# Kernel tuning notes

Hardware: AMD Instinct MI355X
Metric: run time of the kernel (lower is better)

## Reference

```python
import jax, jax.numpy as jnp
import numpy as np

K = 8          # branching factor
D = 4          # tree depth (leaves at depth D)
H = 32         # const node dim
LEAVES = K ** D  # 4096
B = 32
OUT = 2
EPS = 1e-5


def _layer_dims(d):
    # depth d layer: in = (#units at depth d+1), out = (#nodes at d) * H
    n = K ** d
    in_per_child = H if d < D - 1 else 1  # leaf layer feeds scalars
    return n, n * K * in_per_child, n * H, in_per_child


def setup_inputs() -> dict:
    key = jax.random.key(0)
    ks = jax.random.split(key, 64)
    inp = {"x": jax.random.normal(ks[0], (B, LEAVES), jnp.float32)}
    i = 1
    for d in range(D - 1, -1, -1):
        n, fin, fout, ipc = _layer_dims(d)
        # block-diagonal pruning mask: node j rows <- its K children's blocks
        mask = jnp.asarray(np.kron(np.eye(n, dtype=np.float32),
                                   np.ones((H, K * ipc), dtype=np.float32)))
        s = 1.0 / np.sqrt(fin)
        inp[f"Wm{d}"] = jax.random.uniform(ks[i], (fout, fin), jnp.float32, -s, s) * mask; i += 1
        inp[f"bm{d}"] = jax.random.uniform(ks[i], (fout,), jnp.float32, -s, s); i += 1
        inp[f"Wl{d}"] = jax.random.uniform(ks[i], (fout, fin), jnp.float32, -s, s) * mask; i += 1
        inp[f"bl{d}"] = jax.random.uniform(ks[i], (fout,), jnp.float32, -s, s); i += 1
    inp["gate"] = jnp.float32(0.3)
    inp["bn_gamma"] = jnp.ones((H,), jnp.float32)
    inp["bn_beta"] = jnp.zeros((H,), jnp.float32)
    so = 1.0 / np.sqrt(H)
    inp["Wout"] = jax.random.uniform(ks[i], (OUT, H), jnp.float32, -so, so); i += 1
    inp["bout"] = jax.random.uniform(ks[i], (OUT,), jnp.float32, -so, so)
    return inp


def reference(x, Wm3, bm3, Wl3, bl3, Wm2, bm2, Wl2, bl2,
              Wm1, bm1, Wl1, bl1, Wm0, bm0, Wl0, bl0,
              gate, bn_gamma, bn_beta, Wout, bout):
    x_linear = x
    layers = ((Wm3, bm3, Wl3, bl3), (Wm2, bm2, Wl2, bl2),
              (Wm1, bm1, Wl1, bl1), (Wm0, bm0, Wl0, bl0))
    for Wm, bm, Wl, bl in layers:  # depth D-1 -> 0, as in torch forward
        h = jax.nn.relu(x @ Wm.T + bm)          # mlp branch (masked weights)
        x_linear = x_linear @ Wl.T + bl          # parallel linear branch
        x = h * gate + (1.0 - gate) * x_linear   # gated residual combine
    # BatchNorm1d in training mode (biased batch variance)
    mu = jnp.mean(x, axis=0)
    var = jnp.var(x, axis=0)
    xn = (x - mu) * jax.lax.rsqrt(var + EPS)
    y = xn * bn_gamma + bn_beta
    return y @ Wout.T + bout
```

## Files before the change

kernel.cpp:

```cpp
#include <hip/hip_runtime.h>


#define MAGIC 0x5CA1AB1E

__device__ __forceinline__ float dot4(float4 a, float4 b, float acc) {
    acc = fmaf(a.x, b.x, acc);
    acc = fmaf(a.y, b.y, acc);
    acc = fmaf(a.z, b.z, acc);
    acc = fmaf(a.w, b.w, acc);
    return acc;
}
__device__ __forceinline__ float4 ld4(const float* p) { return *(const float4*)p; }

typedef const __attribute__((address_space(1))) void* gas_t;
typedef __attribute__((address_space(3))) void* las_t;

__device__ __forceinline__ void gl_lds16(const float* g, float* l) {
    __builtin_amdgcn_global_load_lds((gas_t)g, (las_t)l, 16, 0, 0);
}

__device__ __forceinline__ void st_xch2(float2* p, float a, float b) {
    union { float2 f2; unsigned long long u; } v;
    v.f2 = make_float2(a, b);
    (void)atomicExch((unsigned long long*)p, v.u);
}
__device__ __forceinline__ float2 ld_wt2(const float2* p) {
    union { float2 f2; unsigned long long u; } v;
    v.u = __hip_atomic_load((const unsigned long long*)p,
                            __ATOMIC_RELAXED, __HIP_MEMORY_SCOPE_AGENT);
    return v.f2;
}
__device__ __forceinline__ void flag_set(int* p) {
    __atomic_signal_fence(__ATOMIC_SEQ_CST);
    __hip_atomic_store(p, MAGIC, __ATOMIC_RELAXED, __HIP_MEMORY_SCOPE_AGENT);
}
__device__ __forceinline__ void flag_wait(const int* p) {
    while (__hip_atomic_load(p, __ATOMIC_RELAXED, __HIP_MEMORY_SCOPE_AGENT) != MAGIC) {}
    __atomic_signal_fence(__ATOMIC_SEQ_CST);
}

__global__ __launch_bounds__(512)
void fused_tree(const float* __restrict__ x,
                const float* __restrict__ Wm3, const float* __restrict__ bm3,
                const float* __restrict__ Wl3, const float* __restrict__ bl3,
                const float* __restrict__ Wm2, const float* __restrict__ bm2,
                const float* __restrict__ Wl2, const float* __restrict__ bl2,
                const float* __restrict__ Wm1, const float* __restrict__ bm1,
                const float* __restrict__ Wl1, const float* __restrict__ bl1,
                const float* __restrict__ Wm0, const float* __restrict__ bm0,
                const float* __restrict__ Wl0, const float* __restrict__ bl0,
                const float* __restrict__ gate_p,
                const float* __restrict__ bn_gamma, const float* __restrict__ bn_beta,
                const float* __restrict__ Wout, const float* __restrict__ bout,
                float2* __restrict__ Qml, float2* __restrict__ Pml,
                int* __restrict__ flags1, int* __restrict__ flags2,
                float* __restrict__ out)
{
    const int blk = blockIdx.x;
    const int j2 = blk & 63, rg = blk >> 6;
    const int tid = threadIdx.x;
    const int wv = tid >> 6, ln = tid & 63;
    const int j1 = j2 >> 3, s = j2 & 7;
    const int cid = rg * 8 + j1;
    const bool is_consumer = (s == 0);

    __shared__ __align__(16) float w2[2][32][260];
    __shared__ __align__(16) float x3[8][260];
    __shared__ __align__(16) float xl3[8][260];
    __shared__ __align__(16) float x2s[8][36];
    __shared__ __align__(16) float xl2s[8][36];
    __shared__ __align__(16) float qm_own[8][36];
    __shared__ __align__(16) float ql_own[8][36];
    __shared__ __align__(16) float x1s[8][36];
    __shared__ __align__(16) float xl1s[8][36];
    __shared__ float x0s[32][33];
    __shared__ float bnm[32], bna[32];
    __shared__ float pW[64], pbo[2], pg[32], pb[32], pbm0[32], pbl0[32];

    const int col = tid & 255, hh3 = tid >> 8;
    const int l3 = col >> 5, t3 = col & 31;
    const int j3 = j2 * 8 + l3;
    const int row3 = j3 * 32 + t3;

    float4 xra[4], xrb[4];
#pragma unroll
    for (int i = 0; i < 4; ++i) {
        const float* xp = x + (size_t)(rg * 8 + hh3 * 4 + i) * 4096 + j3 * 8;
        xra[i] = ld4(xp);
        xrb[i] = ld4(xp + 4);
    }
    const float* wmr = Wm3 + (size_t)row3 * 4096 + j3 * 8;
    const float* wlr = Wl3 + (size_t)row3 * 4096 + j3 * 8;
    const float4 wma = ld4(wmr), wmb = ld4(wmr + 4);
    const float4 wla = ld4(wlr), wlb = ld4(wlr + 4);
    const float bm3v = bm3[row3], bl3v = bl3[row3];
    const float g = gate_p[0], gi = 1.0f - g;

    __builtin_amdgcn_sched_barrier(0);

#pragma unroll
    for (int i = 0; i < 8; ++i) {
        const int q = wv * 8 + i;
        const int m = q >> 5, r = q & 31;
        const float* src = (m ? Wl2 : Wm2)
                         + (size_t)(j2 * 32 + r) * 16384 + j2 * 256 + ln * 4;
        gl_lds16(src, &w2[m][r][0]);
    }
    __builtin_amdgcn_sched_barrier(0);

    const int t2 = tid >> 4;
    const float bm2v = bm2[j2 * 32 + t2];
    const float bl2v = bl2[j2 * 32 + t2];

    const int hp = tid & 1;
    float4 wm1r[4], wl1r[4];
    {
        const float* wr = Wm1 + (size_t)(j1 * 32 + t2) * 2048 + j2 * 32 + hp * 16;
        const float* lr = Wl1 + (size_t)(j1 * 32 + t2) * 2048 + j2 * 32 + hp * 16;
#pragma unroll
        for (int k = 0; k < 4; ++k) {
            wm1r[k] = ld4(wr + k * 4);
            wl1r[k] = ld4(lr + k * 4);
        }
    }

    float4 wm0r[4], wl0r[4];
    float bm1v = 0.0f, bl1v = 0.0f;
    if (is_consumer) {
        const int o2 = tid >> 4;
        const float* p0 = Wm0 + o2 * 256 + j1 * 32 + hp * 16;
        const float* p1 = Wl0 + o2 * 256 + j1 * 32 + hp * 16;
#pragma unroll
        for (int k = 0; k < 4; ++k) {
            wm0r[k] = ld4(p0 + k * 4);
            wl0r[k] = ld4(p1 + k * 4);
        }
        if (tid < 256) {
            bm1v = bm1[j1 * 32 + (tid & 31)];
            bl1v = bl1[j1 * 32 + (tid & 31)];
        }
    }
    if (blk == 0) {
        if (tid < 64) pW[tid] = Wout[tid];
        if (tid < 32) {
            pg[tid]   = bn_gamma[tid];
            pb[tid]   = bn_beta[tid];
            pbm0[tid] = bm0[tid];
            pbl0[tid] = bl0[tid];
        }
        if (tid < 2) pbo[tid] = bout[tid];
    }

#pragma unroll
    for (int i = 0; i < 4; ++i) {
        const int b = hh3 * 4 + i;
        float am = dot4(xra[i], wma, bm3v); am = dot4(xrb[i], wmb, am);
        float al = dot4(xra[i], wla, bl3v); al = dot4(xrb[i], wlb, al);
        x3[b][col]  = fmaf(g, fmaxf(am, 0.0f), gi * al);
        xl3[b][col] = al;
    }
    __syncthreads();

    {
        const int b = (tid >> 1) & 7;
        const float* wmp = &w2[0][t2][hp * 128];
        const float* wlp = &w2[1][t2][hp * 128];
        float pm = 0.0f, pl = 0.0f;
#pragma unroll 8
        for (int c = 0; c < 128; c += 4) {
            pm = dot4(ld4(&x3 [b][hp * 128 + c]), ld4(wmp + c), pm);
            pl = dot4(ld4(&xl3[b][hp * 128 + c]), ld4(wlp + c), pl);
        }
        pm += __shfl_xor(pm, 1);
        pl += __shfl_xor(pl, 1);
        const float am = pm + bm2v, al = pl + bl2v;
        if (hp == 0) x2s [b][t2] = fmaf(g, fmaxf(am, 0.0f), gi * al);
        else         xl2s[b][t2] = al;
    }
    __syncthreads();

    {
        const int b = (tid >> 1) & 7;
        const float* xp = &x2s [b][hp * 16];
        const float* xq = &xl2s[b][hp * 16];
        float pm = 0.0f, pl = 0.0f;
#pragma unroll
        for (int k = 0; k < 4; ++k) {
            pm = dot4(ld4(xp + k * 4), wm1r[k], pm);
            pl = dot4(ld4(xq + k * 4), wl1r[k], pl);
        }
        pm += __shfl_xor(pm, 1);
        pl += __shfl_xor(pl, 1);
        if (is_consumer) {
            if (hp == 0) { qm_own[b][t2] = pm; ql_own[b][t2] = pl; }
        } else if (hp == 0) {
            st_xch2(&Qml[((cid * 8 + s) * 8 + b) * 32 + t2], pm, pl);
        }
    }
    __syncthreads();
    if (!is_consumer) {
        if (tid == 0) flag_set(&flags1[cid * 8 + s]);
        return;
    }

    if (tid < 7) flag_wait(&flags1[cid * 8 + 1 + tid]);
    __syncthreads();

    if (tid < 256) {
        const int b = tid >> 5, t1 = tid & 31;
        float am = bm1v + qm_own[b][t1];
        float al = bl1v + ql_own[b][t1];
#pragma unroll
        for (int t = 1; t < 8; ++t) {
            const float2 q = ld_wt2(&Qml[((cid * 8 + t) * 8 + b) * 32 + t1]);
            am += q.x;
            al += q.y;
        }
        x1s [b][t1] = fmaf(g, fmaxf(am, 0.0f), gi * al);
        xl1s[b][t1] = al;
    }
    __syncthreads();

    {
        const int o2 = tid >> 4, b = (tid >> 1) & 7;
        float pm0 = 0.0f, pl0 = 0.0f;
#pragma unroll
        for (int k = 0; k < 4; ++k) {
            pm0 = dot4(ld4(&x1s [b][hp * 16 + k * 4]), wm0r[k], pm0);
            pl0 = dot4(ld4(&xl1s[b][hp * 16 + k * 4]), wl0r[k], pl0);
        }
        pm0 += __shfl_xor(pm0, 1);
        pl0 += __shfl_xor(pl0, 1);
        if (hp == 0)
            st_xch2(&Pml[j1 * 1024 + (rg * 8 + b) * 32 + o2], pm0, pl0);
    }
    __syncthreads();
    if (blk != 0) {
        if (tid == 0) flag_set(&flags2[cid]);
        return;
    }

    if (tid < 31) flag_wait(&flags2[tid + 1]);
    __syncthreads();

    for (int i = tid; i < 1024; i += 512) {
        const int r = i >> 5, o = i & 31;
        float am = pbm0[o], al = pbl0[o];
#pragma unroll
        for (int j = 0; j < 8; ++j) {
            const float2 p = ld_wt2(&Pml[j * 1024 + r * 32 + o]);
            am += p.x;
            al += p.y;
        }
        x0s[r][o] = fmaf(g, fmaxf(am, 0.0f), gi * al);
    }
    __syncthreads();

    if (tid < 32) {
        float sum = 0.0f, s2 = 0.0f;
#pragma unroll
        for (int r = 0; r < 32; ++r) {
            const float v = x0s[r][tid];
            sum += v;
            s2 = fmaf(v, v, s2);
        }
        const float mu  = sum * (1.0f / 32.0f);
        const float var = s2 * (1.0f / 32.0f) - mu * mu;
        const float m = pg[tid] * rsqrtf(var + 1e-5f);
        bnm[tid] = m;
        bna[tid] = fmaf(-mu, m, pb[tid]);
    }
    __syncthreads();

    if (tid < 64) {
        const int b = tid >> 1, oo = tid & 1;
        float acc = pbo[oo];
#pragma unroll
        for (int t = 0; t < 32; ++t) {
            const float xn = fmaf(x0s[b][t], bnm[t], bna[t]);
            acc = fmaf(xn, pW[oo * 32 + t], acc);
        }
        out[b * 2 + oo] = acc;
    }
}

extern "C" void kernel_launch(void* const* d_in, const int* in_sizes, int n_in,
                              void* d_out, int out_size, void* d_ws, size_t ws_size,
                              hipStream_t stream)
{
    const float* x    = (const float*)d_in[0];
    const float* Wm3  = (const float*)d_in[1];
    const float* bm3  = (const float*)d_in[2];
    const float* Wl3  = (const float*)d_in[3];
    const float* bl3  = (const float*)d_in[4];
    const float* Wm2  = (const float*)d_in[5];
    const float* bm2  = (const float*)d_in[6];
    const float* Wl2  = (const float*)d_in[7];
    const float* bl2  = (const float*)d_in[8];
    const float* Wm1  = (const float*)d_in[9];
    const float* bm1  = (const float*)d_in[10];
    const float* Wl1  = (const float*)d_in[11];
    const float* bl1  = (const float*)d_in[12];
    const float* Wm0  = (const float*)d_in[13];
    const float* bm0  = (const float*)d_in[14];
    const float* Wl0  = (const float*)d_in[15];
    const float* bl0  = (const float*)d_in[16];
    const float* gate = (const float*)d_in[17];
    const float* bn_g = (const float*)d_in[18];
    const float* bn_b = (const float*)d_in[19];
    const float* Wout = (const float*)d_in[20];
    const float* bout = (const float*)d_in[21];
    float* outp = (float*)d_out;

    float*  ws     = (float*)d_ws;
    float2* Qml    = (float2*)ws;
    float2* Pml    = (float2*)(ws + 131072);
    int*    flags1 = (int*)(ws + 147456);
    int*    flags2 = flags1 + 256;

    hipLaunchKernelGGL(fused_tree, dim3(256), dim3(512), 0, stream,
                       x, Wm3, bm3, Wl3, bl3, Wm2, bm2, Wl2, bl2,
                       Wm1, bm1, Wl1, bl1, Wm0, bm0, Wl0, bl0,
                       gate, bn_g, bn_b, Wout, bout,
                       Qml, Pml, flags1, flags2, outp);
}
```

Measured before the change: 17.13 us.

## Repartition blocks by output-row slice across full batch instead of batch groups

Each block now takes the full batch of 32 rows for one depth-2 node and one quarter of its output rows, where before it took 8 batch rows and all 32 outputs. Depth-3 is recomputed for all 32 rows from x staged in LDS through global_load_lds, and each block loads only 8 rows of the depth-2 weights. This cuts the per-block weight traffic and spreads the weight reads across blocks. In exchange, the depth-1 reduction now has one consumer per j1 summing 32 partials instead of 8, the Qml workspace grows, and the flag spin loop gains s_sleep.

```diff
diff --git a/kernel.cpp b/kernel.cpp
--- a/kernel.cpp
+++ b/kernel.cpp
@@ -18,7 +18,9 @@
 __device__ __forceinline__ void gl_lds16(const float* g, float* l) {
     __builtin_amdgcn_global_load_lds((gas_t)g, (las_t)l, 16, 0, 0);
 }
-
+__device__ __forceinline__ void gl_lds4(const float* g, float* l) {
+    __builtin_amdgcn_global_load_lds((gas_t)g, (las_t)l, 4, 0, 0);
+}
 __device__ __forceinline__ void st_xch2(float2* p, float a, float b) {
     union { float2 f2; unsigned long long u; } v;
     v.f2 = make_float2(a, b);
@@ -35,7 +37,8 @@
     __hip_atomic_store(p, MAGIC, __ATOMIC_RELAXED, __HIP_MEMORY_SCOPE_AGENT);
 }
 __device__ __forceinline__ void flag_wait(const int* p) {
-    while (__hip_atomic_load(p, __ATOMIC_RELAXED, __HIP_MEMORY_SCOPE_AGENT) != MAGIC) {}
+    while (__hip_atomic_load(p, __ATOMIC_RELAXED, __HIP_MEMORY_SCOPE_AGENT) != MAGIC)
+        __builtin_amdgcn_s_sleep(1);
     __atomic_signal_fence(__ATOMIC_SEQ_CST);
 }
 
@@ -57,73 +60,73 @@
                 float* __restrict__ out)
 {
     const int blk = blockIdx.x;
-    const int j2 = blk & 63, rg = blk >> 6;
+    const int j1 = blk & 7, s = (blk >> 3) & 7, q = blk >> 6;
+    const int j2 = j1 * 8 + s;
+    const int p  = q * 8 + s;
     const int tid = threadIdx.x;
     const int wv = tid >> 6, ln = tid & 63;
-    const int j1 = j2 >> 3, s = j2 & 7;
-    const int cid = rg * 8 + j1;
-    const bool is_consumer = (s == 0);
-
-    __shared__ __align__(16) float w2[2][32][260];
-    __shared__ __align__(16) float x3[8][260];
-    __shared__ __align__(16) float xl3[8][260];
-    __shared__ __align__(16) float x2s[8][36];
-    __shared__ __align__(16) float xl2s[8][36];
-    __shared__ __align__(16) float qm_own[8][36];
-    __shared__ __align__(16) float ql_own[8][36];
-    __shared__ __align__(16) float x1s[8][36];
-    __shared__ __align__(16) float xl1s[8][36];
+    const bool is_consumer = (p == 0);
+
+    __shared__ __align__(16) float xs[32][64];
+    __shared__ __align__(16) float w2s[2][8][260];
+    __shared__ __align__(16) float x3[32][260];
+    __shared__ __align__(16) float xl3[32][260];
+    __shared__ __align__(16) float x2s[32][12];
+    __shared__ __align__(16) float xl2s[32][12];
+    __shared__ __align__(16) float qm_own[32][36];
+    __shared__ __align__(16) float ql_own[32][36];
+    __shared__ __align__(16) float x1s[32][36];
+    __shared__ __align__(16) float xl1s[32][36];
     __shared__ float x0s[32][33];
     __shared__ float bnm[32], bna[32];
-    __shared__ float pW[64], pbo[2], pg[32], pb[32], pbm0[32], pbl0[32];
-
-    const int col = tid & 255, hh3 = tid >> 8;
-    const int l3 = col >> 5, t3 = col & 31;
-    const int j3 = j2 * 8 + l3;
+    __shared__ float pW[64], pbo[2], pgm[32], pbt[32], pbm0[32], pbl0[32];
+
+    const int col = tid & 255, half = tid >> 8;
+    const int l3i = col >> 5, t3 = col & 31;
+    const int j3 = j2 * 8 + l3i;
     const int row3 = j3 * 32 + t3;
-
-    float4 xra[4], xrb[4];
-#pragma unroll
-    for (int i = 0; i < 4; ++i) {
-        const float* xp = x + (size_t)(rg * 8 + hh3 * 4 + i) * 4096 + j3 * 8;
-        xra[i] = ld4(xp);
-        xrb[i] = ld4(xp + 4);
-    }
     const float* wmr = Wm3 + (size_t)row3 * 4096 + j3 * 8;
     const float* wlr = Wl3 + (size_t)row3 * 4096 + j3 * 8;
     const float4 wma = ld4(wmr), wmb = ld4(wmr + 4);
     const float4 wla = ld4(wlr), wlb = ld4(wlr + 4);
     const float bm3v = bm3[row3], bl3v = bl3[row3];
     const float g = gate_p[0], gi = 1.0f - g;
-
-    __builtin_amdgcn_sched_barrier(0);
-
-#pragma unroll
-    for (int i = 0; i < 8; ++i) {
-        const int q = wv * 8 + i;
-        const int m = q >> 5, r = q & 31;
+    __builtin_amdgcn_sched_barrier(0);
+
+#pragma unroll
+    for (int i = 0; i < 4; ++i) {
+        const int r = wv * 4 + i;
+        gl_lds4(x + (size_t)r * 4096 + j2 * 64 + ln, &xs[r][0]);
+    }
+    __builtin_amdgcn_sched_barrier(0);
+
+#pragma unroll
+    for (int i = 0; i < 2; ++i) {
+        const int idx = wv * 2 + i;
+        const int m = idx >> 3, rl = idx & 7;
         const float* src = (m ? Wl2 : Wm2)
-                         + (size_t)(j2 * 32 + r) * 16384 + j2 * 256 + ln * 4;
-        gl_lds16(src, &w2[m][r][0]);
-    }
-    __builtin_amdgcn_sched_barrier(0);
-
-    const int t2 = tid >> 4;
-    const float bm2v = bm2[j2 * 32 + t2];
-    const float bl2v = bl2[j2 * 32 + t2];
+                         + (size_t)(j2 * 32 + q * 8 + rl) * 16384 + j2 * 256 + ln * 4;
+        gl_lds16(src, &w2s[m][rl][0]);
+    }
+    __builtin_amdgcn_sched_barrier(0);
+    asm volatile("s_waitcnt vmcnt(2)" ::: "memory");
+    __builtin_amdgcn_sched_barrier(0);
+    __builtin_amdgcn_s_barrier();
+    __builtin_amdgcn_sched_barrier(0);
 
     const int hp = tid & 1;
-    float4 wm1r[4], wl1r[4];
+    const int t2l = (tid >> 1) & 7;
+    const float bm2v = bm2[j2 * 32 + q * 8 + t2l];
+    const float bl2v = bl2[j2 * 32 + q * 8 + t2l];
+
+    const int t1 = tid & 31;
+    float4 wm1a, wm1b, wl1a, wl1b;
     {
-        const float* wr = Wm1 + (size_t)(j1 * 32 + t2) * 2048 + j2 * 32 + hp * 16;
-        const float* lr = Wl1 + (size_t)(j1 * 32 + t2) * 2048 + j2 * 32 + hp * 16;
-#pragma unroll
-        for (int k = 0; k < 4; ++k) {
-            wm1r[k] = ld4(wr + k * 4);
-            wl1r[k] = ld4(lr + k * 4);
-        }
-    }
-
+        const float* wr = Wm1 + (size_t)(j1 * 32 + t1) * 2048 + j2 * 32 + q * 8;
+        const float* lr = Wl1 + (size_t)(j1 * 32 + t1) * 2048 + j2 * 32 + q * 8;
+        wm1a = ld4(wr); wm1b = ld4(wr + 4);
+        wl1a = ld4(lr); wl1b = ld4(lr + 4);
+    }
     float4 wm0r[4], wl0r[4];
     float bm1v = 0.0f, bl1v = 0.0f;
     if (is_consumer) {
@@ -135,16 +138,14 @@
             wm0r[k] = ld4(p0 + k * 4);
             wl0r[k] = ld4(p1 + k * 4);
         }
-        if (tid < 256) {
-            bm1v = bm1[j1 * 32 + (tid & 31)];
-            bl1v = bl1[j1 * 32 + (tid & 31)];
-        }
+        bm1v = bm1[j1 * 32 + t1];
+        bl1v = bl1[j1 * 32 + t1];
     }
     if (blk == 0) {
         if (tid < 64) pW[tid] = Wout[tid];
         if (tid < 32) {
-            pg[tid]   = bn_gamma[tid];
-            pb[tid]   = bn_beta[tid];
+            pgm[tid]  = bn_gamma[tid];
+            pbt[tid]  = bn_beta[tid];
             pbm0[tid] = bm0[tid];
             pbl0[tid] = bl0[tid];
         }
@@ -152,69 +153,70 @@
     }
 
 #pragma unroll
-    for (int i = 0; i < 4; ++i) {
-        const int b = hh3 * 4 + i;
-        float am = dot4(xra[i], wma, bm3v); am = dot4(xrb[i], wmb, am);
-        float al = dot4(xra[i], wla, bl3v); al = dot4(xrb[i], wlb, al);
-        x3[b][col]  = fmaf(g, fmaxf(am, 0.0f), gi * al);
-        xl3[b][col] = al;
+    for (int i = 0; i < 16; ++i) {
+        const int r = half * 16 + i;
+        const float4 xa = ld4(&xs[r][l3i * 8]);
+        const float4 xb = ld4(&xs[r][l3i * 8 + 4]);
+        float am = dot4(xa, wma, bm3v); am = dot4(xb, wmb, am);
+        float al = dot4(xa, wla, bl3v); al = dot4(xb, wlb, al);
+        x3[r][col]  = fmaf(g, fmaxf(am, 0.0f), gi * al);
+        xl3[r][col] = al;
     }
     __syncthreads();
 
     {
-        const int b = (tid >> 1) & 7;
-        const float* wmp = &w2[0][t2][hp * 128];
-        const float* wlp = &w2[1][t2][hp * 128];
+        const int b = tid >> 4;
+        const float* wmp = &w2s[0][t2l][hp * 128];
+        const float* wlp = &w2s[1][t2l][hp * 128];
+        const float* xp  = &x3 [b][hp * 128];
+        const float* xq  = &xl3[b][hp * 128];
         float pm = 0.0f, pl = 0.0f;
 #pragma unroll 8
         for (int c = 0; c < 128; c += 4) {
-            pm = dot4(ld4(&x3 [b][hp * 128 + c]), ld4(wmp + c), pm);
-            pl = dot4(ld4(&xl3[b][hp * 128 + c]), ld4(wlp + c), pl);
+            pm = dot4(ld4(xp + c), ld4(wmp + c), pm);
+            pl = dot4(ld4(xq + c), ld4(wlp + c), pl);
         }
         pm += __shfl_xor(pm, 1);
         pl += __shfl_xor(pl, 1);
         const float am = pm + bm2v, al = pl + bl2v;
-        if (hp == 0) x2s [b][t2] = fmaf(g, fmaxf(am, 0.0f), gi * al);
-        else         xl2s[b][t2] = al;
+        if (hp == 0) x2s [b][t2l] = fmaf(g, fmaxf(am, 0.0f), gi * al);
+        else         xl2s[b][t2l] = al;
     }
     __syncthreads();
 
     {
-        const int b = (tid >> 1) & 7;
-        const float* xp = &x2s [b][hp * 16];
-        const float* xq = &xl2s[b][hp * 16];
-        float pm = 0.0f, pl = 0.0f;
-#pragma unroll
-        for (int k = 0; k < 4; ++k) {
-            pm = dot4(ld4(xp + k * 4), wm1r[k], pm);
-            pl = dot4(ld4(xq + k * 4), wl1r[k], pl);
-        }
-        pm += __shfl_xor(pm, 1);
-        pl += __shfl_xor(pl, 1);
-        if (is_consumer) {
-            if (hp == 0) { qm_own[b][t2] = pm; ql_own[b][t2] = pl; }
-        } else if (hp == 0) {
-            st_xch2(&Qml[((cid * 8 + s) * 8 + b) * 32 + t2], pm, pl);
+        const int bb = tid >> 5;
+#pragma unroll
+        for (int i = 0; i < 2; ++i) {
+            const int b = bb * 2 + i;
+            float pm = dot4(ld4(&x2s[b][0]), wm1a, 0.0f);
+            pm       = dot4(ld4(&x2s[b][4]), wm1b, pm);
+            float pl = dot4(ld4(&xl2s[b][0]), wl1a, 0.0f);
+            pl       = dot4(ld4(&xl2s[b][4]), wl1b, pl);
+            if (is_consumer) { qm_own[b][t1] = pm; ql_own[b][t1] = pl; }
+            else st_xch2(&Qml[((j1 * 32 + p) * 32 + b) * 32 + t1], pm, pl);
         }
     }
     __syncthreads();
     if (!is_consumer) {
-        if (tid == 0) flag_set(&flags1[cid * 8 + s]);
+        if (tid == 0) flag_set(&flags1[j1 * 32 + p]);
         return;
     }
 
-    if (tid < 7) flag_wait(&flags1[cid * 8 + 1 + tid]);
-    __syncthreads();
-
-    if (tid < 256) {
-        const int b = tid >> 5, t1 = tid & 31;
+    if (tid < 31) flag_wait(&flags1[j1 * 32 + 1 + tid]);
+    __syncthreads();
+
+#pragma unroll
+    for (int ii = 0; ii < 2; ++ii) {
+        const int idx = ii * 512 + tid;
+        const int b = idx >> 5;
         float am = bm1v + qm_own[b][t1];
         float al = bl1v + ql_own[b][t1];
 #pragma unroll
-        for (int t = 1; t < 8; ++t) {
-            const float2 q = ld_wt2(&Qml[((cid * 8 + t) * 8 + b) * 32 + t1]);
-            am += q.x;
-            al += q.y;
+        for (int t = 1; t < 32; ++t) {
+            const float2 qv = ld_wt2(&Qml[((j1 * 32 + t) * 32 + b) * 32 + t1]);
+            am += qv.x;
+            al += qv.y;
         }
         x1s [b][t1] = fmaf(g, fmaxf(am, 0.0f), gi * al);
         xl1s[b][t1] = al;
@@ -222,35 +224,41 @@
     __syncthreads();
 
     {
-        const int o2 = tid >> 4, b = (tid >> 1) & 7;
-        float pm0 = 0.0f, pl0 = 0.0f;
-#pragma unroll
-        for (int k = 0; k < 4; ++k) {
-            pm0 = dot4(ld4(&x1s [b][hp * 16 + k * 4]), wm0r[k], pm0);
-            pl0 = dot4(ld4(&xl1s[b][hp * 16 + k * 4]), wl0r[k], pl0);
-        }
-        pm0 += __shfl_xor(pm0, 1);
-        pl0 += __shfl_xor(pl0, 1);
-        if (hp == 0)
-            st_xch2(&Pml[j1 * 1024 + (rg * 8 + b) * 32 + o2], pm0, pl0);
+        const int o2 = tid >> 4, bq = (tid >> 1) & 7;
+#pragma unroll
+        for (int i = 0; i < 4; ++i) {
+            const int b = bq + i * 8;
+            float pm0 = 0.0f, pl0 = 0.0f;
+#pragma unroll
+            for (int k = 0; k < 4; ++k) {
+                pm0 = dot4(ld4(&x1s [b][hp * 16 + k * 4]), wm0r[k], pm0);
+                pl0 = dot4(ld4(&xl1s[b][hp * 16 + k * 4]), wl0r[k], pl0);
+            }
+            pm0 += __shfl_xor(pm0, 1);
+            pl0 += __shfl_xor(pl0, 1);
+            if (hp == 0)
+                st_xch2(&Pml[(j1 * 32 + b) * 32 + o2], pm0, pl0);
+        }
     }
     __syncthreads();
     if (blk != 0) {
-        if (tid == 0) flag_set(&flags2[cid]);
+        if (tid == 0) flag_set(&flags2[j1]);
         return;
     }
 
-    if (tid < 31) flag_wait(&flags2[tid + 1]);
-    __syncthreads();
-
-    for (int i = tid; i < 1024; i += 512) {
-        const int r = i >> 5, o = i & 31;
+    if (tid < 7) flag_wait(&flags2[1 + tid]);
+    __syncthreads();
+
+#pragma unroll
+    for (int ii = 0; ii < 2; ++ii) {
+        const int idx = ii * 512 + tid;
+        const int r = idx >> 5, o = idx & 31;
         float am = pbm0[o], al = pbl0[o];
 #pragma unroll
         for (int j = 0; j < 8; ++j) {
-            const float2 p = ld_wt2(&Pml[j * 1024 + r * 32 + o]);
-            am += p.x;
-            al += p.y;
+            const float2 pv = ld_wt2(&Pml[(j * 32 + r) * 32 + o]);
+            am += pv.x;
+            al += pv.y;
         }
         x0s[r][o] = fmaf(g, fmaxf(am, 0.0f), gi * al);
     }
@@ -266,9 +274,9 @@
         }
         const float mu  = sum * (1.0f / 32.0f);
         const float var = s2 * (1.0f / 32.0f) - mu * mu;
-        const float m = pg[tid] * rsqrtf(var + 1e-5f);
+        const float m = pgm[tid] * rsqrtf(var + 1e-5f);
         bnm[tid] = m;
-        bna[tid] = fmaf(-mu, m, pb[tid]);
+        bna[tid] = fmaf(-mu, m, pbt[tid]);
     }
     __syncthreads();
 
@@ -314,8 +322,8 @@
 
     float*  ws     = (float*)d_ws;
     float2* Qml    = (float2*)ws;
-    float2* Pml    = (float2*)(ws + 131072);
-    int*    flags1 = (int*)(ws + 147456);
+    float2* Pml    = (float2*)(ws + 524288);
+    int*    flags1 = (int*)(ws + 540672);
     int*    flags2 = flags1 + 256;
 
     hipLaunchKernelGGL(fused_tree, dim3(256), dim3(512), 0, stream,
```

Result: slower. 24.98 us (+45.8%).
